# Kernel tuning notes

Measured on AMD Instinct MI355X. Metric: run time of the kernel, lower is better.

## Reference

```python
import jax, jax.numpy as jnp
import numpy as np

N_ATOMS = 50000
N_EDGES = 400000
EMB = 256
NUM_RBF = 50
NUM_GATES = 10
F_OUT = 128
BASE_CUTOFF = 0.0
OUTER_CUTOFF = 5.0


def _linear_params(k, din, dout):
    k1, k2 = jax.random.split(k)
    lim = 1.0 / np.sqrt(din)
    W = jax.random.uniform(k1, (din, dout), minval=-lim, maxval=lim, dtype=jnp.float32)
    b = jax.random.uniform(k2, (dout,), minval=-lim, maxval=lim, dtype=jnp.float32)
    return W, b


def setup_inputs() -> dict:
    key = jax.random.key(0)
    ks = jax.random.split(key, 16)
    z = jax.random.randint(ks[0], (N_ATOMS,), 0, 100)
    pos = jax.random.normal(ks[1], (N_ATOMS, 3), dtype=jnp.float32)
    batch = jnp.zeros((N_ATOMS,), dtype=jnp.int32)
    edge_index = jax.random.randint(ks[2], (2, N_EDGES), 0, N_ATOMS)
    edge_vec = jax.random.normal(ks[3], (N_EDGES, 3), dtype=jnp.float32)
    emb_table = jax.random.normal(ks[4], (100, EMB), dtype=jnp.float32)
    W_dist, b_dist = _linear_params(ks[5], NUM_RBF, EMB)
    W_dt, b_dt = _linear_params(ks[6], EMB + 6, EMB)
    W_ai, b_ai = _linear_params(ks[7], EMB, EMB)
    W_aj, b_aj = _linear_params(ks[8], EMB, EMB)
    W_gamma, b_gamma = _linear_params(ks[9], 3 * EMB, EMB)
    lim = 1.0 / np.sqrt(EMB)
    W_exp = jax.random.uniform(ks[10], (NUM_GATES, EMB, F_OUT), minval=-lim, maxval=lim, dtype=jnp.float32)
    b_exp = jax.random.uniform(ks[11], (NUM_GATES, F_OUT), minval=-lim, maxval=lim, dtype=jnp.float32)
    t_params = jax.random.normal(ks[12], (NUM_GATES,), dtype=jnp.float32) * 0.01
    return dict(z=z, pos=pos, batch=batch, edge_index=edge_index, edge_vec=edge_vec,
                emb_table=emb_table, W_dist=W_dist, b_dist=b_dist, W_dt=W_dt, b_dt=b_dt,
                W_ai=W_ai, b_ai=b_ai, W_aj=W_aj, b_aj=b_aj, W_gamma=W_gamma, b_gamma=b_gamma,
                W_exp=W_exp, b_exp=b_exp, t_params=t_params)


def _forward(z, edge_index, edge_vec, emb_table, W_dist, b_dist, W_dt, b_dt,
             W_ai, b_ai, W_aj, b_aj, W_gamma, b_gamma, W_exp, b_exp, t_params):
    x = emb_table[z]                                   # [N, EMB] embedding gather
    d = jnp.linalg.norm(edge_vec, axis=1)              # [E] edge distances
    # Gaussian RBF expansion (torchmd-net GaussianSmearing)
    offset = jnp.linspace(BASE_CUTOFF, OUTER_CUTOFF, NUM_RBF)
    coeff = -0.5 / (offset[1] - offset[0]) ** 2
    edge_attr = jnp.exp(coeff * (d[:, None] - offset[None, :]) ** 2)   # [E, NUM_RBF]
    # CosineCutoff with cutoff_lower == 0
    C = 0.5 * (jnp.cos(d * jnp.pi / OUTER_CUTOFF) + 1.0) * (d < OUTER_CUTOFF).astype(d.dtype)
    ev = edge_vec / d[:, None]                         # normalized edge vectors
    d_proj = (edge_attr @ W_dist + b_dist) * C[:, None]               # [E, EMB]
    feats = jnp.concatenate([d_proj, (d ** 2)[:, None], (d ** 3)[:, None], (d ** 4)[:, None],
                             jnp.sqrt(d)[:, None], jnp.log(d)[:, None], d[:, None]], axis=1)
    d_t = feats @ W_dt + b_dt                          # [E, EMB]
    a_i = x[edge_index[0]] @ W_ai + b_ai               # [E, EMB] gather + linear
    a_j = x[edge_index[1]] @ W_aj + b_aj
    gamma = jnp.concatenate([a_i, a_j, d_t], axis=1) @ W_gamma + b_gamma   # [E, EMB]
    # distance-based expert gate
    gate = jax.nn.softmax(1.0 / jnp.maximum(jnp.abs(d[:, None] - t_params[None, :]), 1e-8), axis=1)  # [E, G]
    edge_out = jnp.zeros((gamma.shape[0], F_OUT), gamma.dtype)
    for g in range(NUM_GATES):                          # small fixed expert loop
        edge_out = edge_out + gate[:, g:g + 1] * (gamma @ W_exp[g] + b_exp[g])
    # scatter to atoms
    atom_out = jax.ops.segment_sum(edge_out, edge_index[0], num_segments=N_ATOMS)   # [N, F_OUT]
    vec = jax.ops.segment_sum(ev[:, :, None] * edge_out[:, None, :], edge_index[0],
                              num_segments=N_ATOMS)                                  # [N, 3, F_OUT]
    return atom_out, vec


def reference(z, pos, batch, edge_index, edge_vec, emb_table, W_dist, b_dist, W_dt, b_dt,
              W_ai, b_ai, W_aj, b_aj, W_gamma, b_gamma, W_exp, b_exp, t_params):
    atom_out, vec = _forward(z, edge_index, edge_vec, emb_table, W_dist, b_dist, W_dt, b_dt,
                             W_ai, b_ai, W_aj, b_aj, W_gamma, b_gamma, W_exp, b_exp, t_params)
    return atom_out, vec, z, pos, batch
```

## Files before the change

kernel.cpp:

```cpp
#include <hip/hip_runtime.h>
#include <math.h>

typedef __bf16 bf16;
typedef __bf16 bf16x8 __attribute__((ext_vector_type(8)));
typedef float  f32x16 __attribute__((ext_vector_type(16)));

#define NATOMS 50000
#define NEDGES 400000
#define NG 10
#define NZ 100
#define BE 128
#define NBLK 3225
#define NLDSC 14
#define DELTA_F 0.10204081632653061f

#define OUT_VEC   6400000LL
#define OUT_Z     25600000LL
#define OUT_POS   25650000LL
#define OUT_BATCH 25800000LL

#define WS_M1   0LL
#define WS_M0   65536LL
#define WS_C0   78336LL
#define WS_M2   78592LL
#define WS_CC   80128LL
#define WS_AI   80384LL
#define WS_AJ   105984LL
#define WS_GI   131584LL
#define WS_GJ   157184LL
#define WS_HI   182784LL
#define WS_HJB  310784LL
#define WS_PTC  413184LL
#define WS_GT   451072LL
#define WS_EV   5404672LL
#define WS_EO   7055872LL
#define WS_I    33475072LL
#define I_CNT   0
#define I_START 50000
#define I_CUR   100000
#define I_CSR   150000
#define I_ZB    550000
#define I_ZC    550128
#define I_B2Z   550256
#define I_BSUM  553488
#define I_BOFF  553552
#define I_PERM  553616


__device__ __forceinline__ float dot256(const float* __restrict__ a,
                                        const float* __restrict__ B, int c)
{
    float s0 = 0, s1 = 0, s2 = 0, s3 = 0;
    for (int k = 0; k < 256; k += 4) {
        s0 += a[k]     * B[(k)     * 256 + c];
        s1 += a[k + 1] * B[(k + 1) * 256 + c];
        s2 += a[k + 2] * B[(k + 2) * 256 + c];
        s3 += a[k + 3] * B[(k + 3) * 256 + c];
    }
    return (s0 + s1) + (s2 + s3);
}

__device__ __forceinline__ unsigned pack2bf(float a, float b)
{
    union { __bf16 h; unsigned short u; } ca, cb;
    ca.h = (__bf16)a; cb.h = (__bf16)b;
    return (unsigned)ca.u | ((unsigned)cb.u << 16);
}


__global__ void kA(const float* __restrict__ W_dt, const float* __restrict__ b_dt,
                   const float* __restrict__ b_gamma, const float* __restrict__ Wg3,
                   float* __restrict__ M1, float* __restrict__ M2, float* __restrict__ cc,
                   const float* __restrict__ emb,
                   const float* __restrict__ W_ai, const float* __restrict__ b_ai,
                   const float* __restrict__ W_aj, const float* __restrict__ b_aj,
                   float* __restrict__ Ai, float* __restrict__ Aj,
                   const int* __restrict__ esrc, const int* __restrict__ edst,
                   const int* __restrict__ z,
                   int* __restrict__ cnt, int* __restrict__ zbins,
                   const float* __restrict__ pos, const int* __restrict__ batch,
                   float* __restrict__ out)
{
    const int r = blockIdx.x, tid = threadIdx.x;
    if (r < 263) {
        const float* a = (r < 262) ? (W_dt + (size_t)r * 256) : b_dt;
        float res = dot256(a, Wg3, tid);
        if (r == 262) res += b_gamma[tid];
        if (r < 256) M1[(size_t)r * 256 + tid] = res;
        else if (r < 262) M2[(size_t)(r - 256) * 256 + tid] = res;
        else cc[tid] = res;
    } else if (r < 463) {
        const int r2 = r - 263;
        const int zz = r2 % 100, side = r2 / 100;
        float res = dot256(emb + (size_t)zz * 256, side ? W_aj : W_ai, tid)
                  + (side ? b_aj[tid] : b_ai[tid]);
        (side ? Aj : Ai)[(size_t)zz * 256 + tid] = res;
    } else if (r < 2026) {
        __shared__ int h[NZ];
        for (int i = tid; i < NZ; i += 256) h[i] = 0;
        __syncthreads();
        const int e = (r - 463) * 256 + tid;
        if (e < NEDGES) {
            atomicAdd(&cnt[esrc[e]], 1);
            atomicAdd(&h[z[edst[e]]], 1);
        }
        __syncthreads();
        for (int i = tid; i < NZ; i += 256) if (h[i]) atomicAdd(&zbins[i], h[i]);
    } else {
        const int i = (r - 2026) * 256 + tid;
        if (i < NATOMS) {
            out[OUT_Z + i] = (float)z[i];
            out[OUT_BATCH + i] = (float)batch[i];
        }
        if (i < 3 * NATOMS) out[OUT_POS + i] = pos[i];
    }
}


__global__ void kB(const float* __restrict__ W_dist, const float* __restrict__ b_dist,
                   const float* __restrict__ M1, float* __restrict__ M0, float* __restrict__ c0,
                   const float* __restrict__ Ai, const float* __restrict__ Aj,
                   const float* __restrict__ Wg1, const float* __restrict__ Wg2,
                   float* __restrict__ Gi, float* __restrict__ Gj)
{
    const int r = blockIdx.x, c = threadIdx.x;
    if (r < 51) {
        const float* a = (r < 50) ? (W_dist + (size_t)r * 256) : b_dist;
        float res = dot256(a, M1, c);
        if (r < 50) M0[(size_t)r * 256 + c] = res; else c0[c] = res;
    } else {
        const int r2 = r - 51;
        const int zz = r2 % 100, side = r2 / 100;
        float res = side ? dot256(Aj + (size_t)zz * 256, Wg2, c)
                         : dot256(Ai + (size_t)zz * 256, Wg1, c);
        (side ? Gj : Gi)[(size_t)zz * 256 + c] = res;
    }
}


__global__ void kC(const float* __restrict__ Gi, const float* __restrict__ Gj,
                   const float* __restrict__ Wexp,
                   float* __restrict__ Hi, bf16* __restrict__ Hjb,
                   const float* __restrict__ M0, const float* __restrict__ M2,
                   const float* __restrict__ c0, const float* __restrict__ cc,
                   const float* __restrict__ b_exp, bf16* __restrict__ PTc)
{
    const int r = blockIdx.x;
    const int f = threadIdx.x;
    if (r < 1000) {
        const int zz = r / 10, g = r - zz * 10;
        const float* w  = Wexp + (size_t)g * 32768 + f;
        const float* gi = Gi + (size_t)zz * 256;
        const float* gj = Gj + (size_t)zz * 256;
        float a0=0,a1=0,a2=0,a3=0,b0=0,b1=0,b2=0,b3=0;
        for (int k = 0; k < 256; k += 4) {
            const float w0 = w[k*128], w1 = w[(k+1)*128], w2 = w[(k+2)*128], w3 = w[(k+3)*128];
            a0 += gi[k]*w0;   a1 += gi[k+1]*w1; a2 += gi[k+2]*w2; a3 += gi[k+3]*w3;
            b0 += gj[k]*w0;   b1 += gj[k+1]*w1; b2 += gj[k+2]*w2; b3 += gj[k+3]*w3;
        }
        Hi[(size_t)r * 128 + f] = (a0+a1)+(a2+a3);
        Hjb[(size_t)zz * 2048 + (g >> 3) * 1024 + f * 8 + (g & 7)] = (bf16)((b0+b1)+(b2+b3));
    } else {
        const int b = r - 1000;
        const int ck = b >> 4, kl = b & 15;
        const int k = ck * 16 + kl;
        float val = 0.f;
        if (k < 580) {
            const float* arow; int g; float bias = 0.f;
            if (k < 500)      { g = k / 50; arow = M0 + (size_t)(k - g * 50) * 256; }
            else if (k < 560) { const int jj = k - 500; g = jj / 6; arow = M2 + (size_t)(jj - g * 6) * 256; }
            else if (k < 570) { g = k - 560; arow = c0; }
            else              { g = k - 570; arow = cc; bias = b_exp[g * 128 + f]; }
            const float* w = Wexp + (size_t)g * 32768 + f;
            float s0=0,s1=0,s2=0,s3=0;
            for (int c2 = 0; c2 < 256; c2 += 4) {
                s0 += arow[c2]   * w[(c2)   * 128];
                s1 += arow[c2+1] * w[(c2+1) * 128];
                s2 += arow[c2+2] * w[(c2+2) * 128];
                s3 += arow[c2+3] * w[(c2+3) * 128];
            }
            val = (s0+s1)+(s2+s3) + bias;
        }
        PTc[(size_t)ck * 2048 + (kl >> 3) * 1024 + f * 8 + (kl & 7)] = (bf16)val;
    }
}


__global__ void kD1(const int* __restrict__ cnt, int* __restrict__ startp,
                    int* __restrict__ bsum)
{
    __shared__ int part[1024];
    const int tid = threadIdx.x;
    const int i = blockIdx.x * 1024 + tid;
    const int v = (i < NATOMS) ? cnt[i] : 0;
    part[tid] = v;
    __syncthreads();
    for (int off = 1; off < 1024; off <<= 1) {
        int t2 = part[tid];
        if (tid >= off) t2 += part[tid - off];
        __syncthreads();
        part[tid] = t2;
        __syncthreads();
    }
    if (i < NATOMS) startp[i] = part[tid] - v;
    if (tid == 1023) bsum[blockIdx.x] = part[1023];
}

__global__ void kD2(const int* __restrict__ bsum, int* __restrict__ boffs,
                    const int* __restrict__ zbins, int* __restrict__ zcursor,
                    int* __restrict__ blk2z)
{
    __shared__ int sc[256];
    const int tid = threadIdx.x;
    const int v = (tid < 49) ? bsum[tid] : 0;
    sc[tid] = v;
    __syncthreads();
    for (int off = 1; off < 64; off <<= 1) {
        int t2 = sc[tid];
        if (tid >= off) t2 += sc[tid - off];
        __syncthreads();
        sc[tid] = t2;
        __syncthreads();
    }
    if (tid < 49) boffs[tid] = sc[tid] - v;
    __syncthreads();
    const int pz = (tid < NZ) ? (((zbins[tid] + 127) >> 7) << 7) : 0;
    sc[tid] = pz;
    __syncthreads();
    for (int off = 1; off < 128; off <<= 1) {
        int t2 = sc[tid];
        if (tid >= off) t2 += sc[tid - off];
        __syncthreads();
        sc[tid] = t2;
        __syncthreads();
    }
    if (tid < NZ) {
        const int st = sc[tid] - pz;
        zcursor[tid] = st;
        for (int b = (st >> 7); b < (sc[tid] >> 7); ++b) blk2z[b] = tid;
    }
}

__global__ void kD3(const int* __restrict__ boffs, int* __restrict__ startp,
                    int* __restrict__ cursor)
{
    const int i = blockIdx.x * 1024 + threadIdx.x;
    if (i < NATOMS) {
        const int s2 = startp[i] + boffs[blockIdx.x];
        startp[i] = s2;
        cursor[i] = s2;
    }
}

#define ZF_EPB 1024
__global__ void __launch_bounds__(256) k_zfill(
    const int* __restrict__ edst, const int* __restrict__ z,
    const int* __restrict__ esrc,
    int* __restrict__ zcursor, int* __restrict__ cursor,
    int* __restrict__ perm, int* __restrict__ csr)
{
    __shared__ int h[NZ];
    __shared__ int base[NZ];
    const int t = threadIdx.x;
    for (int i = t; i < NZ; i += 256) h[i] = 0;
    __syncthreads();
    const int e0 = blockIdx.x * ZF_EPB;
    int rank[4], zb[4];
#pragma unroll
    for (int k2 = 0; k2 < 4; ++k2) {
        const int e = e0 + t + k2 * 256;
        if (e < NEDGES) { zb[k2] = z[edst[e]]; rank[k2] = atomicAdd(&h[zb[k2]], 1); }
        else zb[k2] = -1;
    }
    __syncthreads();
    for (int i = t; i < NZ; i += 256) base[i] = h[i] ? atomicAdd(&zcursor[i], h[i]) : 0;
    __syncthreads();
#pragma unroll
    for (int k2 = 0; k2 < 4; ++k2) {
        if (zb[k2] >= 0) {
            const int e = e0 + t + k2 * 256;
            const int pos = base[zb[k2]] + rank[k2];
            perm[pos] = e;
            const int p2 = atomicAdd(&cursor[esrc[e]], 1);
            csr[p2] = pos;
        }
    }
}


__device__ __forceinline__ float coeff(int k, const unsigned* Gp, const float* gate,
                                       const float* sv, float C)
{
    if (k < 500) {
        const int g = k / 50, rb = k - g * 50;
        const unsigned w = Gp[rb >> 1];
        const unsigned bits = (rb & 1) ? (w & 0xffff0000u) : (w << 16);
        return gate[g] * __uint_as_float(bits);
    } else if (k < 560) {
        const int jj = k - 500;
        return gate[jj / 6] * sv[jj - (jj / 6) * 6];
    } else if (k < 570) {
        return C * gate[k - 560];
    } else if (k < 580) {
        return gate[k - 570];
    }
    return 0.0f;
}

__global__ void __launch_bounds__(256, 2) k_edge(
    const float* __restrict__ edge_vec,
    const int* __restrict__ perm, const int* __restrict__ blk2z,
    const float* __restrict__ tpar,
    const bf16* __restrict__ PTc, const bf16* __restrict__ Hjb,
    float* __restrict__ gates_ws, float* __restrict__ evb, bf16* __restrict__ eo)
{
    __shared__ __align__(16) bf16 Bs[(NLDSC + 1) * 2048];

    const int t    = threadIdx.x;
    const int wid  = t >> 6;
    const int lane = t & 63;
    const int er   = lane & 31;
    const int kh   = lane >> 5;
    const bool khb = (kh != 0);
    const int base = blockIdx.x * BE;
    const int pid  = base + wid * 32 + er;

    if (perm[base] < 0) return;

    const int zb  = blk2z[blockIdx.x];
    const int eid = perm[pid];

    const float4* PTc4 = (const float4*)PTc;
    float4 stg[NLDSC];
#pragma unroll
    for (int i = 0; i < NLDSC; ++i) stg[i] = PTc4[t + i * 256];
    const float4 hv = ((const float4*)(Hjb + (size_t)zb * 2048))[t];

    float gate[NG], sv[6];
    float d = 1.0f, C = 0.0f, vx = 0.f, vy = 0.f, vz = 0.f;
    if (eid >= 0) {
        vx = edge_vec[eid * 3]; vy = edge_vec[eid * 3 + 1]; vz = edge_vec[eid * 3 + 2];
        d = sqrtf(vx * vx + vy * vy + vz * vz);
        C = (d < 5.0f) ? 0.5f * (__cosf(d * 0.6283185307179586f) + 1.0f) : 0.0f;
        float m = -3.0e38f;
#pragma unroll
        for (int g = 0; g < NG; ++g) {
            float r = 1.0f / fmaxf(fabsf(d - tpar[g]), 1e-8f);
            gate[g] = r; m = fmaxf(m, r);
        }
        float ss = 0.f;
#pragma unroll
        for (int g = 0; g < NG; ++g) { float ex = __expf(gate[g] - m); gate[g] = ex; ss += ex; }
        const float inv = 1.0f / ss;
#pragma unroll
        for (int g = 0; g < NG; ++g) gate[g] *= inv;
        const float d2 = d * d;
        sv[0] = d2; sv[1] = d2 * d; sv[2] = d2 * d2;
        sv[3] = sqrtf(d); sv[4] = __logf(d); sv[5] = d;
    } else {
#pragma unroll
        for (int g = 0; g < NG; ++g) gate[g] = 0.f;
#pragma unroll
        for (int m2 = 0; m2 < 6; ++m2) sv[m2] = 0.f;
    }

    unsigned Gp[25];
#pragma unroll
    for (int p = 0; p < 25; ++p) {
        const float t0 = d - (float)(2 * p) * DELTA_F;
        const float t1 = t0 - DELTA_F;
        const float g0 = C * __expf(-48.02f * t0 * t0);
        const float g1 = C * __expf(-48.02f * t1 * t1);
        Gp[p] = pack2bf(g0, g1);
    }

    if (kh == 0 && eid >= 0) {
        float* gw = gates_ws + (size_t)pid * 12;
#pragma unroll
        for (int g = 0; g < NG; ++g) gw[g] = gate[g];
        const float invd = 1.0f / d;
        *(float4*)(evb + (size_t)pid * 4) =
            make_float4(vx * invd, vy * invd, vz * invd, 0.0f);
    }

    {
        float4* dst = (float4*)Bs;
#pragma unroll
        for (int i = 0; i < NLDSC; ++i) dst[t + i * 256] = stg[i];
        dst[t + NLDSC * 256] = hv;
    }
    __syncthreads();

    f32x16 acc0 = {}, acc1 = {}, acc2 = {}, acc3 = {};
    const int lanoff = kh * 1024 + er * 8;
    const bf16* Lp = Bs + lanoff;
    const bf16* Gb = PTc + lanoff;

#define MFMA4(AV, B0, B1, B2, B3) do { \
        acc0 = __builtin_amdgcn_mfma_f32_32x32x16_bf16(AV, B0, acc0, 0, 0, 0); \
        acc1 = __builtin_amdgcn_mfma_f32_32x32x16_bf16(AV, B1, acc1, 0, 0, 0); \
        acc2 = __builtin_amdgcn_mfma_f32_32x32x16_bf16(AV, B2, acc2, 0, 0, 0); \
        acc3 = __builtin_amdgcn_mfma_f32_32x32x16_bf16(AV, B3, acc3, 0, 0, 0); \
    } while (0)
#define LDB(P, V0, V1, V2, V3) \
        const bf16x8 V0 = *(const bf16x8*)(P); \
        const bf16x8 V1 = *(const bf16x8*)((P) + 256); \
        const bf16x8 V2 = *(const bf16x8*)((P) + 512); \
        const bf16x8 V3 = *(const bf16x8*)((P) + 768);

    {
        bf16x8 av;
#pragma unroll
        for (int j = 0; j < 8; ++j) {
            const float va = gate[j];
            const float vb = (j < 2) ? gate[8 + j] : 0.0f;
            av[j] = (bf16)(khb ? vb : va);
        }
        LDB(Lp + NLDSC * 2048, b0, b1, b2, b3);
        MFMA4(av, b0, b1, b2, b3);
    }

    bf16x8 c0, c1, c2, c3, n0, n1, n2, n3;
    {
        const bf16* bp = Gb + NLDSC * 2048;
        c0 = *(const bf16x8*)(bp);       c1 = *(const bf16x8*)(bp + 256);
        c2 = *(const bf16x8*)(bp + 512); c3 = *(const bf16x8*)(bp + 768);
    }
    {
        const bf16* bp = Gb + (NLDSC + 1) * 2048;
        n0 = *(const bf16x8*)(bp);       n1 = *(const bf16x8*)(bp + 256);
        n2 = *(const bf16x8*)(bp + 512); n3 = *(const bf16x8*)(bp + 768);
    }

#pragma unroll
    for (int ks = 0; ks < NLDSC; ++ks) {
        bf16x8 av;
#pragma unroll
        for (int j = 0; j < 8; ++j) {
            const float va = coeff(ks * 16 + j,     Gp, gate, sv, C);
            const float vb = coeff(ks * 16 + 8 + j, Gp, gate, sv, C);
            av[j] = (bf16)(khb ? vb : va);
        }
        LDB(Lp + ks * 2048, b0, b1, b2, b3);
        MFMA4(av, b0, b1, b2, b3);
    }

#pragma unroll
    for (int ks = NLDSC; ks < 37; ++ks) {
        const bf16x8 m0 = c0, m1 = c1, m2 = c2, m3 = c3;
        c0 = n0; c1 = n1; c2 = n2; c3 = n3;
        if (ks + 2 <= 36) {
            const bf16* bp = Gb + (size_t)(ks + 2) * 2048;
            n0 = *(const bf16x8*)(bp);       n1 = *(const bf16x8*)(bp + 256);
            n2 = *(const bf16x8*)(bp + 512); n3 = *(const bf16x8*)(bp + 768);
        }
        bf16x8 av;
#pragma unroll
        for (int j = 0; j < 8; ++j) {
            const float va = coeff(ks * 16 + j,     Gp, gate, sv, C);
            const float vb = coeff(ks * 16 + 8 + j, Gp, gate, sv, C);
            av[j] = (bf16)(khb ? vb : va);
        }
        MFMA4(av, m0, m1, m2, m3);
    }
#undef MFMA4
#undef LDB

    bf16* eor = eo + (size_t)(base + wid * 32) * 128 + er;
#pragma unroll
    for (int r = 0; r < 16; ++r) {
        const int crow = (r & 3) + 8 * (r >> 2) + 4 * kh;
        bf16* p = eor + (size_t)crow * 128;
        p[0]  = (bf16)acc0[r];
        p[32] = (bf16)acc1[r];
        p[64] = (bf16)acc2[r];
        p[96] = (bf16)acc3[r];
    }
}


__global__ void __launch_bounds__(256) k_gather(
    const bf16* __restrict__ eo, const float* __restrict__ evb,
    const float* __restrict__ gates_ws,
    const int* __restrict__ startp, const int* __restrict__ cnt,
    const int* __restrict__ csr, const int* __restrict__ zarr,
    const float* __restrict__ Hi, float* __restrict__ out)
{
    const int atom = blockIdx.x * 4 + (threadIdx.x >> 6);
    const int lane = threadIdx.x & 63;
    if (atom >= NATOMS) return;
    const int s = startp[atom], len = cnt[atom];
    const unsigned* eo32 = (const unsigned*)eo;
    const float4* ev4 = (const float4*)evb;
    const float4* gq  = (const float4*)gates_ws;
    float a0 = 0, a1 = 0, v00 = 0, v01 = 0, v10 = 0, v11 = 0, v20 = 0, v21 = 0;
    float gs[NG] = {}, e0g[NG] = {}, e1g[NG] = {}, e2g[NG] = {};

#define ACCE(EV, QA, QB, QC, U) do { \
        const float ga_[NG] = {QA.x, QA.y, QA.z, QA.w, QB.x, QB.y, QB.z, QB.w, QC.x, QC.y}; \
        _Pragma("unroll") \
        for (int g = 0; g < NG; ++g) { \
            gs[g] += ga_[g]; e0g[g] += EV.x * ga_[g]; \
            e1g[g] += EV.y * ga_[g]; e2g[g] += EV.z * ga_[g]; \
        } \
        const float y0 = __uint_as_float(U << 16); \
        const float y1 = __uint_as_float(U & 0xffff0000u); \
        a0 += y0; a1 += y1; \
        v00 += EV.x * y0; v01 += EV.x * y1; \
        v10 += EV.y * y0; v11 += EV.y * y1; \
        v20 += EV.z * y0; v21 += EV.z * y1; \
    } while (0)

    int i = 0;
    for (; i + 4 <= len; i += 4) {
        const int p0 = csr[s + i],     p1 = csr[s + i + 1];
        const int p2 = csr[s + i + 2], p3 = csr[s + i + 3];
        const float4 e0 = ev4[p0], e1 = ev4[p1], e2 = ev4[p2], e3 = ev4[p3];
        const unsigned u0 = eo32[(size_t)p0 * 64 + lane];
        const unsigned u1 = eo32[(size_t)p1 * 64 + lane];
        const unsigned u2 = eo32[(size_t)p2 * 64 + lane];
        const unsigned u3 = eo32[(size_t)p3 * 64 + lane];
        const float4 qa0 = gq[(size_t)p0 * 3], qb0 = gq[(size_t)p0 * 3 + 1], qc0 = gq[(size_t)p0 * 3 + 2];
        const float4 qa1 = gq[(size_t)p1 * 3], qb1 = gq[(size_t)p1 * 3 + 1], qc1 = gq[(size_t)p1 * 3 + 2];
        const float4 qa2 = gq[(size_t)p2 * 3], qb2 = gq[(size_t)p2 * 3 + 1], qc2 = gq[(size_t)p2 * 3 + 2];
        const float4 qa3 = gq[(size_t)p3 * 3], qb3 = gq[(size_t)p3 * 3 + 1], qc3 = gq[(size_t)p3 * 3 + 2];
        ACCE(e0, qa0, qb0, qc0, u0);
        ACCE(e1, qa1, qb1, qc1, u1);
        ACCE(e2, qa2, qb2, qc2, u2);
        ACCE(e3, qa3, qb3, qc3, u3);
    }
    for (; i < len; ++i) {
        const int p0 = csr[s + i];
        const float4 e0 = ev4[p0];
        const unsigned u0 = eo32[(size_t)p0 * 64 + lane];
        const float4 qa0 = gq[(size_t)p0 * 3], qb0 = gq[(size_t)p0 * 3 + 1], qc0 = gq[(size_t)p0 * 3 + 2];
        ACCE(e0, qa0, qb0, qc0, u0);
    }
#undef ACCE

    const float* Hrow = Hi + (size_t)zarr[atom] * 1280;
#pragma unroll
    for (int g = 0; g < NG; ++g) {
        const float2 h2 = *(const float2*)(Hrow + g * 128 + 2 * lane);
        a0  += gs[g] * h2.x;  a1  += gs[g] * h2.y;
        v00 += e0g[g] * h2.x; v01 += e0g[g] * h2.y;
        v10 += e1g[g] * h2.x; v11 += e1g[g] * h2.y;
        v20 += e2g[g] * h2.x; v21 += e2g[g] * h2.y;
    }
    float* ao = out + (size_t)atom * 128;
    *(float2*)(ao + 2 * lane) = make_float2(a0, a1);
    float* vp = out + OUT_VEC + (size_t)atom * 384;
    *(float2*)(vp + 2 * lane)       = make_float2(v00, v01);
    *(float2*)(vp + 128 + 2 * lane) = make_float2(v10, v11);
    *(float2*)(vp + 256 + 2 * lane) = make_float2(v20, v21);
}


extern "C" void kernel_launch(void* const* d_in, const int* in_sizes, int n_in,
                              void* d_out, int out_size, void* d_ws, size_t ws_size,
                              hipStream_t stream)
{
    const int*   z        = (const int*)d_in[0];
    const float* pos      = (const float*)d_in[1];
    const int*   batch    = (const int*)d_in[2];
    const int*   esrc     = (const int*)d_in[3];
    const int*   edst     = esrc + NEDGES;
    const float* edge_vec = (const float*)d_in[4];
    const float* emb      = (const float*)d_in[5];
    const float* W_dist   = (const float*)d_in[6];
    const float* b_dist   = (const float*)d_in[7];
    const float* W_dt     = (const float*)d_in[8];
    const float* b_dt     = (const float*)d_in[9];
    const float* W_ai     = (const float*)d_in[10];
    const float* b_ai     = (const float*)d_in[11];
    const float* W_aj     = (const float*)d_in[12];
    const float* b_aj     = (const float*)d_in[13];
    const float* W_gamma  = (const float*)d_in[14];
    const float* b_gamma  = (const float*)d_in[15];
    const float* W_exp    = (const float*)d_in[16];
    const float* b_exp    = (const float*)d_in[17];
    const float* tpar     = (const float*)d_in[18];

    float* out = (float*)d_out;
    float* W   = (float*)d_ws;

    const float* Wg1 = W_gamma;
    const float* Wg2 = W_gamma + 256 * 256;
    const float* Wg3 = W_gamma + 512 * 256;

    float* M1 = W + WS_M1;
    float* M0 = W + WS_M0;
    float* c0 = W + WS_C0;
    float* M2 = W + WS_M2;
    float* cc = W + WS_CC;
    float* Ai = W + WS_AI;
    float* Aj = W + WS_AJ;
    float* Gi = W + WS_GI;
    float* Gj = W + WS_GJ;
    float* Hi = W + WS_HI;
    bf16*  Hjb = (bf16*)(W + WS_HJB);
    bf16*  PTc = (bf16*)(W + WS_PTC);
    float* gates = W + WS_GT;
    float* evb   = W + WS_EV;
    bf16*  eo    = (bf16*)(W + WS_EO);
    int*   I     = (int*)(W + WS_I);
    int* cnt    = I + I_CNT;
    int* startp = I + I_START;
    int* cursor = I + I_CUR;
    int* csr    = I + I_CSR;
    int* zbins  = I + I_ZB;
    int* zcur   = I + I_ZC;
    int* b2z    = I + I_B2Z;
    int* bsum   = I + I_BSUM;
    int* boffs  = I + I_BOFF;
    int* perm   = I + I_PERM;

    hipMemsetAsync(cnt, 0, NATOMS * sizeof(int), stream);
    hipMemsetAsync(zbins, 0, 128 * sizeof(int), stream);
    hipMemsetAsync(perm, 0xFF, (size_t)NBLK * BE * sizeof(int), stream);
    hipMemsetAsync(Hjb, 0, 100 * 2048 * sizeof(bf16), stream);

    kA<<<2613, 256, 0, stream>>>(W_dt, b_dt, b_gamma, Wg3, M1, M2, cc,
                                 emb, W_ai, b_ai, W_aj, b_aj, Ai, Aj,
                                 esrc, edst, z, cnt, zbins, pos, batch, out);
    kB<<<251, 256, 0, stream>>>(W_dist, b_dist, M1, M0, c0, Ai, Aj, Wg1, Wg2, Gi, Gj);
    kC<<<1592, 128, 0, stream>>>(Gi, Gj, W_exp, Hi, Hjb, M0, M2, c0, cc, b_exp, PTc);
    kD1<<<49, 1024, 0, stream>>>(cnt, startp, bsum);
    kD2<<<1, 256, 0, stream>>>(bsum, boffs, zbins, zcur, b2z);
    kD3<<<49, 1024, 0, stream>>>(boffs, startp, cursor);
    k_zfill<<<(NEDGES + ZF_EPB - 1) / ZF_EPB, 256, 0, stream>>>(edst, z, esrc, zcur, cursor, perm, csr);

    k_edge<<<NBLK, 256, 0, stream>>>(edge_vec, perm, b2z, tpar, PTc, Hjb, gates, evb, eo);
    k_gather<<<(NATOMS + 3) / 4, 256, 0, stream>>>(eo, evb, gates, startp, cnt, csr, z, Hi, out);
}
```

Before: 291.9 us.

## Double edge block size to 256 and distribute gate accumulation across lanes in gather

The edge kernel now processes 256 edges per block with 512 threads, so each block's shared-memory load of the PTc and Hj weight slab serves twice as many edges and fewer blocks are launched. Padding per z-bin grows to 256, which adds more wasted padded edges, and the workspace offsets are shifted to match. In the gather kernel, the per-lane 40-float gate and vector-gate accumulations are replaced by one accumulator per lane for the first 40 lanes, reduced through shared memory. This cuts redundant gate loads and register pressure. The new shared-memory exchange has no barrier, but it stays inside a single wavefront.

```diff
diff --git a/kernel.cpp b/kernel.cpp
--- a/kernel.cpp
+++ b/kernel.cpp
@@ -9,9 +9,9 @@
 #define NEDGES 400000
 #define NG 10
 #define NZ 100
-#define BE 128
-#define NBLK 3225
-#define NLDSC 14
+#define BE 256
+#define NBLK 1700
+#define NLDSC 15
 #define DELTA_F 0.10204081632653061f
 
 #define OUT_VEC   6400000LL
@@ -32,9 +32,9 @@
 #define WS_HJB  310784LL
 #define WS_PTC  413184LL
 #define WS_GT   451072LL
-#define WS_EV   5404672LL
-#define WS_EO   7055872LL
-#define WS_I    33475072LL
+#define WS_EV   5673472LL
+#define WS_EO   7414272LL
+#define WS_I    35267072LL
 #define I_CNT   0
 #define I_START 50000
 #define I_CUR   100000
@@ -42,9 +42,9 @@
 #define I_ZB    550000
 #define I_ZC    550128
 #define I_B2Z   550256
-#define I_BSUM  553488
-#define I_BOFF  553552
-#define I_PERM  553616
+#define I_BSUM  551956
+#define I_BOFF  552020
+#define I_PERM  552084
 
 
 __device__ __forceinline__ float dot256(const float* __restrict__ a,
@@ -224,7 +224,7 @@
     }
     if (tid < 49) boffs[tid] = sc[tid] - v;
     __syncthreads();
-    const int pz = (tid < NZ) ? (((zbins[tid] + 127) >> 7) << 7) : 0;
+    const int pz = (tid < NZ) ? (((zbins[tid] + 255) >> 8) << 8) : 0;
     sc[tid] = pz;
     __syncthreads();
     for (int off = 1; off < 128; off <<= 1) {
@@ -237,7 +237,7 @@
     if (tid < NZ) {
         const int st = sc[tid] - pz;
         zcursor[tid] = st;
-        for (int b = (st >> 7); b < (sc[tid] >> 7); ++b) blk2z[b] = tid;
+        for (int b = (st >> 8); b < (sc[tid] >> 8); ++b) blk2z[b] = tid;
     }
 }
 
@@ -307,7 +307,7 @@
     return 0.0f;
 }
 
-__global__ void __launch_bounds__(256, 2) k_edge(
+__global__ void __launch_bounds__(512, 2) k_edge(
     const float* __restrict__ edge_vec,
     const int* __restrict__ perm, const int* __restrict__ blk2z,
     const float* __restrict__ tpar,
@@ -331,10 +331,11 @@
     const int eid = perm[pid];
 
     const float4* PTc4 = (const float4*)PTc;
-    float4 stg[NLDSC];
-#pragma unroll
-    for (int i = 0; i < NLDSC; ++i) stg[i] = PTc4[t + i * 256];
-    const float4 hv = ((const float4*)(Hjb + (size_t)zb * 2048))[t];
+    const float4* Hj4  = (const float4*)(Hjb + (size_t)zb * 2048);
+    float4 stg[8];
+#pragma unroll
+    for (int i = 0; i < 7; ++i) stg[i] = PTc4[t + i * 512];
+    stg[7] = (t < 256) ? PTc4[3584 + t] : Hj4[t - 256];
 
     float gate[NG], sv[6];
     float d = 1.0f, C = 0.0f, vx = 0.f, vy = 0.f, vz = 0.f;
@@ -386,8 +387,8 @@
     {
         float4* dst = (float4*)Bs;
 #pragma unroll
-        for (int i = 0; i < NLDSC; ++i) dst[t + i * 256] = stg[i];
-        dst[t + NLDSC * 256] = hv;
+        for (int i = 0; i < 7; ++i) dst[t + i * 512] = stg[i];
+        dst[3584 + t] = stg[7];
     }
     __syncthreads();
 
@@ -486,25 +487,27 @@
     const int* __restrict__ csr, const int* __restrict__ zarr,
     const float* __restrict__ Hi, float* __restrict__ out)
 {
-    const int atom = blockIdx.x * 4 + (threadIdx.x >> 6);
+    __shared__ float gsum[4][48];
+    const int wloc = threadIdx.x >> 6;
+    const int atom = blockIdx.x * 4 + wloc;
     const int lane = threadIdx.x & 63;
     if (atom >= NATOMS) return;
     const int s = startp[atom], len = cnt[atom];
     const unsigned* eo32 = (const unsigned*)eo;
     const float4* ev4 = (const float4*)evb;
-    const float4* gq  = (const float4*)gates_ws;
+
+    const int comp = lane / 10;
+    const int gidx = lane - comp * 10;
+    const bool gl = (lane < 40);
+    float gacc = 0.0f;
+
     float a0 = 0, a1 = 0, v00 = 0, v01 = 0, v10 = 0, v11 = 0, v20 = 0, v21 = 0;
-    float gs[NG] = {}, e0g[NG] = {}, e1g[NG] = {}, e2g[NG] = {};
-
-#define ACCE(EV, QA, QB, QC, U) do { \
-        const float ga_[NG] = {QA.x, QA.y, QA.z, QA.w, QB.x, QB.y, QB.z, QB.w, QC.x, QC.y}; \
-        _Pragma("unroll") \
-        for (int g = 0; g < NG; ++g) { \
-            gs[g] += ga_[g]; e0g[g] += EV.x * ga_[g]; \
-            e1g[g] += EV.y * ga_[g]; e2g[g] += EV.z * ga_[g]; \
-        } \
-        const float y0 = __uint_as_float(U << 16); \
-        const float y1 = __uint_as_float(U & 0xffff0000u); \
+
+#define ACCE(PID, EV, U) do { \
+        const float evc = (comp == 1) ? EV.x : (comp == 2) ? EV.y : (comp == 3) ? EV.z : 1.0f; \
+        if (gl) gacc += evc * gates_ws[(size_t)(PID) * 12 + gidx]; \
+        const float y0 = __uint_as_float((U) << 16); \
+        const float y1 = __uint_as_float((U) & 0xffff0000u); \
         a0 += y0; a1 += y1; \
         v00 += EV.x * y0; v01 += EV.x * y1; \
         v10 += EV.y * y0; v11 += EV.y * y1; \
@@ -520,32 +523,33 @@
         const unsigned u1 = eo32[(size_t)p1 * 64 + lane];
         const unsigned u2 = eo32[(size_t)p2 * 64 + lane];
         const unsigned u3 = eo32[(size_t)p3 * 64 + lane];
-        const float4 qa0 = gq[(size_t)p0 * 3], qb0 = gq[(size_t)p0 * 3 + 1], qc0 = gq[(size_t)p0 * 3 + 2];
-        const float4 qa1 = gq[(size_t)p1 * 3], qb1 = gq[(size_t)p1 * 3 + 1], qc1 = gq[(size_t)p1 * 3 + 2];
-        const float4 qa2 = gq[(size_t)p2 * 3], qb2 = gq[(size_t)p2 * 3 + 1], qc2 = gq[(size_t)p2 * 3 + 2];
-        const float4 qa3 = gq[(size_t)p3 * 3], qb3 = gq[(size_t)p3 * 3 + 1], qc3 = gq[(size_t)p3 * 3 + 2];
-        ACCE(e0, qa0, qb0, qc0, u0);
-        ACCE(e1, qa1, qb1, qc1, u1);
-        ACCE(e2, qa2, qb2, qc2, u2);
-        ACCE(e3, qa3, qb3, qc3, u3);
+        ACCE(p0, e0, u0);
+        ACCE(p1, e1, u1);
+        ACCE(p2, e2, u2);
+        ACCE(p3, e3, u3);
     }
     for (; i < len; ++i) {
         const int p0 = csr[s + i];
         const float4 e0 = ev4[p0];
         const unsigned u0 = eo32[(size_t)p0 * 64 + lane];
-        const float4 qa0 = gq[(size_t)p0 * 3], qb0 = gq[(size_t)p0 * 3 + 1], qc0 = gq[(size_t)p0 * 3 + 2];
-        ACCE(e0, qa0, qb0, qc0, u0);
+        ACCE(p0, e0, u0);
     }
 #undef ACCE
 
+    if (gl) gsum[wloc][comp * 10 + gidx] = gacc;
+
     const float* Hrow = Hi + (size_t)zarr[atom] * 1280;
 #pragma unroll
     for (int g = 0; g < NG; ++g) {
+        const float gs = gsum[wloc][g];
+        const float e0 = gsum[wloc][10 + g];
+        const float e1 = gsum[wloc][20 + g];
+        const float e2 = gsum[wloc][30 + g];
         const float2 h2 = *(const float2*)(Hrow + g * 128 + 2 * lane);
-        a0  += gs[g] * h2.x;  a1  += gs[g] * h2.y;
-        v00 += e0g[g] * h2.x; v01 += e0g[g] * h2.y;
-        v10 += e1g[g] * h2.x; v11 += e1g[g] * h2.y;
-        v20 += e2g[g] * h2.x; v21 += e2g[g] * h2.y;
+        a0  += gs * h2.x;  a1  += gs * h2.y;
+        v00 += e0 * h2.x;  v01 += e0 * h2.y;
+        v10 += e1 * h2.x;  v11 += e1 * h2.y;
+        v20 += e2 * h2.x;  v21 += e2 * h2.y;
     }
     float* ao = out + (size_t)atom * 128;
     *(float2*)(ao + 2 * lane) = make_float2(a0, a1);
@@ -630,6 +634,6 @@
     kD3<<<49, 1024, 0, stream>>>(boffs, startp, cursor);
     k_zfill<<<(NEDGES + ZF_EPB - 1) / ZF_EPB, 256, 0, stream>>>(edst, z, esrc, zcur, cursor, perm, csr);
 
-    k_edge<<<NBLK, 256, 0, stream>>>(edge_vec, perm, b2z, tpar, PTc, Hjb, gates, evb, eo);
+    k_edge<<<NBLK, 512, 0, stream>>>(edge_vec, perm, b2z, tpar, PTc, Hjb, gates, evb, eo);
     k_gather<<<(NATOMS + 3) / 4, 256, 0, stream>>>(eo, evb, gates, startp, cnt, csr, z, Hi, out);
 }
```

After: 283.8 us. -2.8%, faster.
